# Kernel tuning notes

Measured on AMD Instinct MI355X. Metric: run time of the kernel, lower is better.

Reference implementation:

```python
import math
import jax, jax.numpy as jnp
import numpy as np

VOCAB, D, H, L, DFF, MAXLEN, PAD = 32000, 512, 8, 6, 2048, 5000, 0
DK = D // H
EPS = 1e-5


def _positional_encoding(max_len, d_model):
    pos = np.arange(max_len, dtype=np.float32)[:, None]
    div = np.exp(np.arange(0, d_model, 2, dtype=np.float32) * (-math.log(10000.0) / d_model))
    pe = np.zeros((max_len, d_model), dtype=np.float32)
    pe[:, 0::2] = np.sin(pos * div)
    pe[:, 1::2] = np.cos(pos * div)
    return jnp.asarray(pe)


def setup_inputs() -> dict:
    key = jax.random.key(0)
    ks = jax.random.split(key, 16)
    B, S = 2, 2048
    src = jax.random.randint(ks[0], (B, S), 0, VOCAB)
    emb = jax.random.normal(ks[1], (VOCAB, D), jnp.float32) * (D ** -0.5)
    emb = emb.at[PAD].set(0.0)  # padding_idx row zeroed
    pe = _positional_encoding(MAXLEN, D)
    s = 0.02
    WQ = jax.random.normal(ks[2], (L, D, D), jnp.float32) * s
    WK = jax.random.normal(ks[3], (L, D, D), jnp.float32) * s
    WV = jax.random.normal(ks[4], (L, D, D), jnp.float32) * s
    WO = jax.random.normal(ks[5], (L, D, D), jnp.float32) * s
    W1 = jax.random.normal(ks[6], (L, D, DFF), jnp.float32) * s
    b1 = jnp.zeros((L, DFF), jnp.float32)
    W2 = jax.random.normal(ks[7], (L, DFF, D), jnp.float32) * s
    b2 = jnp.zeros((L, D), jnp.float32)
    ln1_s = jnp.ones((L, D), jnp.float32); ln1_b = jnp.zeros((L, D), jnp.float32)
    ln2_s = jnp.ones((L, D), jnp.float32); ln2_b = jnp.zeros((L, D), jnp.float32)
    fn_s = jnp.ones((D,), jnp.float32); fn_b = jnp.zeros((D,), jnp.float32)
    return dict(src=src, emb=emb, pe=pe, WQ=WQ, WK=WK, WV=WV, WO=WO,
                W1=W1, b1=b1, W2=W2, b2=b2, ln1_s=ln1_s, ln1_b=ln1_b,
                ln2_s=ln2_s, ln2_b=ln2_b, fn_s=fn_s, fn_b=fn_b)


def _layernorm(x, scale, bias):
    mu = jnp.mean(x, axis=-1, keepdims=True)
    var = jnp.mean(jnp.square(x - mu), axis=-1, keepdims=True)
    return (x - mu) * jax.lax.rsqrt(var + EPS) * scale + bias


def _encoder_forward(src, emb, pe, WQ, WK, WV, WO, W1, b1, W2, b2,
                     ln1_s, ln1_b, ln2_s, ln2_b, fn_s, fn_b):
    B, S = src.shape
    key_mask = (src != PAD)[:, None, None, :]  # [B,1,1,S] padding mask
    x = emb[src] * math.sqrt(D) + pe[:S]        # [B,S,D] (dropout=eval/off)
    for l in range(L):
        # --- pre-LN self-attention ---
        h = _layernorm(x, ln1_s[l], ln1_b[l])
        q = (h @ WQ[l]).reshape(B, S, H, DK).transpose(0, 2, 1, 3)
        k = (h @ WK[l]).reshape(B, S, H, DK).transpose(0, 2, 1, 3)
        v = (h @ WV[l]).reshape(B, S, H, DK).transpose(0, 2, 1, 3)
        scores = jnp.einsum('bhqd,bhkd->bhqk', q, k) / math.sqrt(DK)
        scores = jnp.where(key_mask, scores, -jnp.inf)
        w = jax.nn.softmax(scores, axis=-1)
        w = jnp.nan_to_num(w, nan=0.0)
        attn = jnp.einsum('bhqk,bhkd->bhqd', w, v)
        attn = attn.transpose(0, 2, 1, 3).reshape(B, S, D) @ WO[l]
        x = x + attn
        # --- pre-LN FFN ---
        h = _layernorm(x, ln2_s[l], ln2_b[l])
        h = jax.nn.relu(h @ W1[l] + b1[l]) @ W2[l] + b2[l]
        x = x + h
    return _layernorm(x, fn_s, fn_b)


def reference(src, emb, pe, WQ, WK, WV, WO, W1, b1, W2, b2,
              ln1_s, ln1_b, ln2_s, ln2_b, fn_s, fn_b):
    return _encoder_forward(src, emb, pe, WQ, WK, WV, WO, W1, b1, W2, b2,
                            ln1_s, ln1_b, ln2_s, ln2_b, fn_s, fn_b)
```

## Files before the change

### kernel.cpp

```cpp
#include <hip/hip_runtime.h>


typedef _Float16 f16;
typedef _Float16 f16x8 __attribute__((ext_vector_type(8)));
typedef _Float16 f16x4 __attribute__((ext_vector_type(4)));
typedef float    f32x4 __attribute__((ext_vector_type(4)));

#define MFMA16(a, b, c) __builtin_amdgcn_mfma_f32_16x16x32_f16((a), (b), (c), 0, 0, 0)
#define GLOAD_LDS16(GP, LP)                                        \
  __builtin_amdgcn_global_load_lds(                                \
      (const __attribute__((address_space(1))) void*)(GP),         \
      (__attribute__((address_space(3))) void*)(LP), 16, 0, 0)

__device__ inline float fast_exp2(float x) {
#if __has_builtin(__builtin_amdgcn_exp2f)
  return __builtin_amdgcn_exp2f(x);
#else
  return exp2f(x);
#endif
}

static constexpr int Dm  = 512;
static constexpr int Sx  = 2048;
static constexpr int NTOK = 4096;
static constexpr int DFFm = 2048;
static constexpr int Lc  = 6;

__global__ __launch_bounds__(256) void transpose_qkvo(
    const float* __restrict__ WQ, const float* __restrict__ WK,
    const float* __restrict__ WV, const float* __restrict__ WO,
    f16* __restrict__ wqkv, f16* __restrict__ wtO)
{
  __shared__ float t[32][33];
  const int z = blockIdx.z;
  const int widx = z / 6, layer = z % 6;
  const float* src = ((widx == 0) ? WQ : (widx == 1) ? WK : (widx == 2) ? WV : WO)
                     + (size_t)layer * Dm * Dm;
  f16* dst = (widx < 3)
      ? wqkv + (size_t)layer * 1536 * Dm + (size_t)widx * 512 * Dm
      : wtO + (size_t)layer * Dm * Dm;
  const int r0 = blockIdx.y * 32, c0 = blockIdx.x * 32;
  const int tx = threadIdx.x, ty = threadIdx.y;
  #pragma unroll
  for (int i = 0; i < 4; i++)
    t[ty + i * 8][tx] = src[(size_t)(r0 + ty + i * 8) * Dm + c0 + tx];
  __syncthreads();
  #pragma unroll
  for (int i = 0; i < 4; i++)
    dst[(size_t)(c0 + ty + i * 8) * Dm + r0 + tx] = (f16)t[tx][ty + i * 8];
}

__global__ __launch_bounds__(256) void transpose_cvt(
    const float* __restrict__ in, f16* __restrict__ out, int R, int C, size_t zs)
{
  __shared__ float t[32][33];
  const int z = blockIdx.z;
  const float* src = in + (size_t)z * zs;
  f16* dst = out + (size_t)z * zs;
  const int r0 = blockIdx.y * 32, c0 = blockIdx.x * 32;
  const int tx = threadIdx.x, ty = threadIdx.y;
  #pragma unroll
  for (int i = 0; i < 4; i++)
    t[ty + i * 8][tx] = src[(size_t)(r0 + ty + i * 8) * C + c0 + tx];
  __syncthreads();
  #pragma unroll
  for (int i = 0; i < 4; i++)
    dst[(size_t)(c0 + ty + i * 8) * R + r0 + tx] = (f16)t[tx][ty + i * 8];
}

__global__ __launch_bounds__(256) void embed_k(
    const int* __restrict__ src, const float* __restrict__ emb,
    const float* __restrict__ pe, float* __restrict__ x, float* __restrict__ mb)
{
  const int gid = blockIdx.x * 256 + threadIdx.x;
  const int token = gid >> 6;
  const int d0 = (gid & 63) << 3;
  const int s = token & (Sx - 1);
  const int tk = src[token];
  if ((gid & 63) == 0) mb[token] = (tk != 0) ? 0.f : -3.0e38f;
  const float* e = emb + (size_t)tk * Dm + d0;
  const float* p = pe + (size_t)s * Dm + d0;
  float* o = x + (size_t)token * Dm + d0;
  const float SC = 22.627416997969522f;
  #pragma unroll
  for (int j = 0; j < 8; j++) o[j] = e[j] * SC + p[j];
}

template <typename OUT, int ADD, int BIAS, int WRITEX>
__global__ __launch_bounds__(256) void lnf_k(
    const float* __restrict__ x, const f16* __restrict__ part,
    const float* __restrict__ bias,
    const float* __restrict__ sc, const float* __restrict__ bi,
    OUT* __restrict__ out, float* __restrict__ xout)
{
  const int row = blockIdx.x * 4 + (threadIdx.x >> 6);
  const int l = threadIdx.x & 63;
  const float* px = x + (size_t)row * Dm + l * 8;
  float v[8];
  *(float4*)&v[0] = *(const float4*)px;
  *(float4*)&v[4] = *(const float4*)(px + 4);
  if constexpr (ADD) {
    f16x8 p = *(const f16x8*)(part + (size_t)row * Dm + l * 8);
    #pragma unroll
    for (int j = 0; j < 8; j++) v[j] += (float)p[j];
    if constexpr (BIAS) {
      float bb[8];
      *(float4*)&bb[0] = *(const float4*)(bias + l * 8);
      *(float4*)&bb[4] = *(const float4*)(bias + l * 8 + 4);
      #pragma unroll
      for (int j = 0; j < 8; j++) v[j] += bb[j];
    }
    if constexpr (WRITEX) {
      float* pxo = xout + (size_t)row * Dm + l * 8;
      *(float4*)pxo = *(const float4*)&v[0];
      *(float4*)(pxo + 4) = *(const float4*)&v[4];
    }
  }
  float s = 0.f;
  #pragma unroll
  for (int j = 0; j < 8; j++) s += v[j];
  #pragma unroll
  for (int m = 1; m < 64; m <<= 1) s += __shfl_xor(s, m);
  const float mu = s * (1.0f / 512.0f);
  float qv = 0.f;
  #pragma unroll
  for (int j = 0; j < 8; j++) { float d = v[j] - mu; qv += d * d; }
  #pragma unroll
  for (int m = 1; m < 64; m <<= 1) qv += __shfl_xor(qv, m);
  const float inv = rsqrtf(qv * (1.0f / 512.0f) + 1e-5f);
  float scv[8], biv[8];
  *(float4*)&scv[0] = *(const float4*)(sc + l * 8);
  *(float4*)&scv[4] = *(const float4*)(sc + l * 8 + 4);
  *(float4*)&biv[0] = *(const float4*)(bi + l * 8);
  *(float4*)&biv[4] = *(const float4*)(bi + l * 8 + 4);
  if constexpr (sizeof(OUT) == 2) {
    f16x8 o;
    #pragma unroll
    for (int j = 0; j < 8; j++) o[j] = (f16)((v[j] - mu) * inv * scv[j] + biv[j]);
    *(f16x8*)((f16*)out + (size_t)row * Dm + l * 8) = o;
  } else {
    float o[8];
    #pragma unroll
    for (int j = 0; j < 8; j++) o[j] = (v[j] - mu) * inv * scv[j] + biv[j];
    float* po = (float*)out + (size_t)row * Dm + l * 8;
    *(float4*)po = *(float4*)&o[0];
    *(float4*)(po + 4) = *(float4*)&o[4];
  }
}

template <int BN, int MODE, int N, int K>
__global__ __launch_bounds__(256) void gemm_k(
    const f16* __restrict__ A, const f16* __restrict__ Bt,
    f16* __restrict__ O0, f16* __restrict__ O1, f16* __restrict__ O2,
    const float* __restrict__ bias)
{
  constexpr int BM = 128;
  constexpr int NF = (BN >= 32) ? BN / 32 : 1;
  constexpr int NBM = NTOK / BM;
  constexpr int NBN = N / BN;
  constexpr int NB = NBM * NBN;
  __shared__ f16 lsA[2][BM * 64];
  __shared__ f16 lsB[2][BN * 64];
  const int tid = threadIdx.x;
  const int l = tid & 63, w = tid >> 6;
  const int lr = l & 15, lh = l >> 4;
  const int wm = w >> 1, wn = w & 1;
  const int bid = blockIdx.x;
  const int nid = (bid & 7) * (NB / 8) + (bid >> 3);
  const int bm = nid / NBN, bn = nid % NBN;

  constexpr int ACH = (BM * 64) / (256 * 8);
  constexpr int BCH = (BN * 64) / (256 * 8);
  const size_t rowA0 = (size_t)bm * BM;
  const size_t rowB0 = (size_t)bn * BN;

  auto stage = [&](int kt, int pb) {
    #pragma unroll
    for (int i = 0; i < ACH; i++) {
      int c = i * 256 + tid, r = c >> 3, g = c & 7, gs = g ^ (r & 7);
      GLOAD_LDS16(A + (rowA0 + r) * K + kt * 64 + gs * 8, &lsA[pb][c * 8]);
    }
    #pragma unroll
    for (int i = 0; i < BCH; i++) {
      int c = i * 256 + tid, r = c >> 3, g = c & 7, gs = g ^ (r & 7);
      GLOAD_LDS16(Bt + (rowB0 + r) * K + kt * 64 + gs * 8, &lsB[pb][c * 8]);
    }
  };

  f32x4 acc[4][NF] = {};
  stage(0, 0);
  constexpr int NT = K >> 6;
  for (int kt = 0; kt < NT; ++kt) {
    const int cur = kt & 1;
    __syncthreads();
    if (kt + 1 < NT) stage(kt + 1, cur ^ 1);
    #pragma unroll
    for (int s = 0; s < 2; s++) {
      const int gg = (s * 4 + lh) ^ (lr & 7);
      f16x8 af[4], bf[NF];
      #pragma unroll
      for (int mf = 0; mf < 4; mf++)
        af[mf] = *(const f16x8*)(&lsA[cur][(wm * 64 + mf * 16 + lr) * 64 + gg * 8]);
      #pragma unroll
      for (int nf = 0; nf < NF; nf++)
        bf[nf] = *(const f16x8*)(&lsB[cur][(wn * (BN / 2) + nf * 16 + lr) * 64 + gg * 8]);
      #pragma unroll
      for (int mf = 0; mf < 4; mf++)
        #pragma unroll
        for (int nf = 0; nf < NF; nf++)
          acc[mf][nf] = MFMA16(af[mf], bf[nf], acc[mf][nf]);
    }
  }

  #pragma unroll
  for (int mf = 0; mf < 4; mf++) {
    #pragma unroll
    for (int nf = 0; nf < NF; nf++) {
      const int token = bm * BM + wm * 64 + mf * 16 + lh * 4;
      const int ch = bn * BN + wn * (BN / 2) + nf * 16 + lr;
      if constexpr (MODE == 0) {
        const int part = ch >> 9;
        const int pch = ch & 511;
        if (part == 2) {
          f16x4 o;
          #pragma unroll
          for (int r = 0; r < 4; r++) o[r] = (f16)acc[mf][nf][r];
          const int bb = token >> 11, ss = token & (Sx - 1);
          const int scol = (ss & ~31) | (((ss >> 2) & 3) << 3) | (((ss >> 4) & 1) << 2);
          *(f16x4*)(O2 + ((size_t)((bb << 3) + (pch >> 6)) * 64 + (pch & 63)) * Sx + scol) = o;
        } else {
          f16* Oz = (part == 0) ? O0 : O1;
          #pragma unroll
          for (int r = 0; r < 4; r++)
            Oz[(size_t)(token + r) * Dm + pch] = (f16)acc[mf][nf][r];
        }
      } else if constexpr (MODE == 1) {
        #pragma unroll
        for (int r = 0; r < 4; r++)
          O0[(size_t)(token + r) * N + ch] = (f16)acc[mf][nf][r];
      } else {
        #pragma unroll
        for (int r = 0; r < 4; r++) {
          float v = acc[mf][nf][r] + bias[ch];
          O0[(size_t)(token + r) * N + ch] = (f16)fmaxf(v, 0.f);
        }
      }
    }
  }
}

__global__ __launch_bounds__(512) void attn_k(
    const f16* __restrict__ q, const f16* __restrict__ kk,
    const f16* __restrict__ vt, const float* __restrict__ maskb,
    f16* __restrict__ out)
{
  __shared__ f16 lsK[2][2][64 * 64];
  __shared__ f16 lsV[2][2][64 * 64];
  const int tid = threadIdx.x;
  const int l = tid & 63, w = tid >> 6;
  const int lr = l & 15, lh = l >> 4;
  const int grp = w >> 2;
  const int t256 = tid & 255;
  const int bid = blockIdx.x;
  const int nid = ((bid & 7) << 6) + (bid >> 3);
  const int bh = nid >> 5;
  const int qt = nid & 31;
  const int b = bh >> 3, h = bh & 7;

  const _Float16 QS = (_Float16)0.18033688f;
  f16x8 qf[2];
  #pragma unroll
  for (int s = 0; s < 2; s++) {
    size_t row = (size_t)(b * Sx + qt * 64 + (w & 3) * 16 + lr);
    f16x8 t = *(const f16x8*)(q + row * Dm + h * 64 + s * 32 + lh * 8);
    qf[s] = t * QS;
  }

  const f16x8 ones = {(f16)1, (f16)1, (f16)1, (f16)1,
                      (f16)1, (f16)1, (f16)1, (f16)1};
  f32x4 oacc[4] = {};
  f32x4 sumacc = {};
  float mrun = -1e30f;

  auto stage = [&](int t, int pb) {
    #pragma unroll
    for (int i = 0; i < 2; i++) {
      int c = i * 256 + t256, r = c >> 3, g = c & 7, gs = g ^ (r & 7);
      GLOAD_LDS16(kk + (size_t)(b * Sx + t * 64 + r) * Dm + h * 64 + gs * 8,
                  &lsK[grp][pb][c * 8]);
      GLOAD_LDS16(vt + (size_t)(bh * 64 + r) * Sx + t * 64 + gs * 8,
                  &lsV[grp][pb][c * 8]);
    }
  };
  stage(grp * 16, 0);

  for (int i = 0; i < 16; ++i) {
    const int t = grp * 16 + i;
    const int cur = i & 1;
    __syncthreads();
    if (i < 15) stage(t + 1, cur ^ 1);

    f32x4 sacc[4];
    #pragma unroll
    for (int kf = 0; kf < 4; kf++)
      sacc[kf] = *(const f32x4*)(maskb + b * Sx + t * 64 + kf * 16 + lh * 4);
    __builtin_amdgcn_s_setprio(1);
    #pragma unroll
    for (int s = 0; s < 2; s++) {
      const int gk = (s * 4 + lh) ^ (lr & 7);
      #pragma unroll
      for (int kf = 0; kf < 4; kf++) {
        f16x8 a = *(const f16x8*)(&lsK[grp][cur][(kf * 16 + lr) * 64 + gk * 8]);
        sacc[kf] = MFMA16(a, qf[s], sacc[kf]);
      }
    }
    __builtin_amdgcn_s_setprio(0);

    float pmax;
    {
      float t0 = fmaxf(fmaxf(sacc[0][0], sacc[0][1]), sacc[0][2]);
      float t1 = fmaxf(fmaxf(sacc[0][3], sacc[1][0]), sacc[1][1]);
      float t2 = fmaxf(fmaxf(sacc[1][2], sacc[1][3]), sacc[2][0]);
      float t3 = fmaxf(fmaxf(sacc[2][1], sacc[2][2]), sacc[2][3]);
      float t4 = fmaxf(fmaxf(sacc[3][0], sacc[3][1]), sacc[3][2]);
      float u0 = fmaxf(fmaxf(t0, t1), sacc[3][3]);
      float u1 = fmaxf(fmaxf(t2, t3), t4);
      pmax = fmaxf(u0, u1);
    }
    pmax = fmaxf(pmax, __shfl_xor(pmax, 16));
    pmax = fmaxf(pmax, __shfl_xor(pmax, 32));
    if (!__all(pmax - mrun <= 8.0f)) {
      const float mnew = fmaxf(mrun, pmax);
      const float rs = fast_exp2(mrun - mnew);
      sumacc *= rs;
      #pragma unroll
      for (int mf = 0; mf < 4; mf++) oacc[mf] *= rs;
      mrun = mnew;
    }
    #pragma unroll
    for (int kf = 0; kf < 4; kf++)
      #pragma unroll
      for (int r = 0; r < 4; r++)
        sacc[kf][r] = fast_exp2(sacc[kf][r] - mrun);
    f16x8 pa[2];
    #pragma unroll
    for (int s = 0; s < 2; s++)
      #pragma unroll
      for (int jj = 0; jj < 8; jj++)
        pa[s][jj] = (f16)sacc[2 * s + (jj >> 2)][jj & 3];
    sumacc = MFMA16(ones, pa[0], sumacc);
    sumacc = MFMA16(ones, pa[1], sumacc);

    __builtin_amdgcn_s_setprio(1);
    #pragma unroll
    for (int s = 0; s < 2; s++) {
      const int gv = (4 * s + lh) ^ (lr & 7);
      #pragma unroll
      for (int mf = 0; mf < 4; mf++) {
        f16x8 vv = *(const f16x8*)(&lsV[grp][cur][(mf * 16 + lr) * 64 + gv * 8]);
        oacc[mf] = MFMA16(vv, pa[s], oacc[mf]);
      }
    }
    __builtin_amdgcn_s_setprio(0);
  }

  const float lrun = sumacc[0];
  __syncthreads();
  float* sO  = (float*)&lsK[0][0][0];
  float* sML = (float*)&lsV[0][0][0];
  const int wl = (w & 3) * 64 + l;
  if (grp == 1) {
    #pragma unroll
    for (int mf = 0; mf < 4; mf++)
      #pragma unroll
      for (int r = 0; r < 4; r++) sO[wl * 16 + mf * 4 + r] = oacc[mf][r];
    sML[wl * 2] = mrun;
    sML[wl * 2 + 1] = lrun;
  }
  __syncthreads();
  if (grp == 0) {
    const float m1 = sML[wl * 2], l1 = sML[wl * 2 + 1];
    const float mm = fmaxf(mrun, m1);
    const float s0 = fast_exp2(mrun - mm), s1 = fast_exp2(m1 - mm);
    const float inv = 1.f / (lrun * s0 + l1 * s1);
    size_t row = (size_t)(b * Sx + qt * 64 + (w & 3) * 16 + lr);
    #pragma unroll
    for (int mf = 0; mf < 4; mf++) {
      f16x4 o;
      #pragma unroll
      for (int r = 0; r < 4; r++)
        o[r] = (f16)((oacc[mf][r] * s0 + sO[wl * 16 + mf * 4 + r] * s1) * inv);
      *(f16x4*)(out + row * Dm + h * 64 + mf * 16 + lh * 4) = o;
    }
  }
}

extern "C" void kernel_launch(void* const* d_in, const int* in_sizes, int n_in,
                              void* d_out, int out_size, void* d_ws, size_t ws_size,
                              hipStream_t stream)
{
  (void)in_sizes; (void)n_in; (void)out_size; (void)ws_size;
  const int*   src  = (const int*)d_in[0];
  const float* emb  = (const float*)d_in[1];
  const float* pe   = (const float*)d_in[2];
  const float* WQ   = (const float*)d_in[3];
  const float* WK   = (const float*)d_in[4];
  const float* WV   = (const float*)d_in[5];
  const float* WO   = (const float*)d_in[6];
  const float* W1   = (const float*)d_in[7];
  const float* b1   = (const float*)d_in[8];
  const float* W2   = (const float*)d_in[9];
  const float* b2   = (const float*)d_in[10];
  const float* ln1s = (const float*)d_in[11];
  const float* ln1b = (const float*)d_in[12];
  const float* ln2s = (const float*)d_in[13];
  const float* ln2b = (const float*)d_in[14];
  const float* fns  = (const float*)d_in[15];
  const float* fnb  = (const float*)d_in[16];

  char* ws = (char*)d_ws;
  const size_t DD = (size_t)Dm * Dm;
  const size_t DQKV = (size_t)1536 * Dm;
  const size_t DF = (size_t)Dm * DFFm;
  f16* wqkv = (f16*)(ws);
  f16* wtO  = wqkv + Lc * DQKV;
  f16* wt1  = wtO + Lc * DD;
  f16* wt2  = wt1 + Lc * DF;
  float* x  = (float*)(wt2 + Lc * DF);
  f16* hbuf = (f16*)(x + (size_t)NTOK * Dm);
  f16* qb   = hbuf + (size_t)NTOK * Dm;
  f16* kb   = qb + (size_t)NTOK * Dm;
  f16* vtb  = kb + (size_t)NTOK * Dm;
  f16* attn = vtb + (size_t)NTOK * Dm;
  f16* aout = attn + (size_t)NTOK * Dm;
  f16* ff   = aout + (size_t)NTOK * Dm;
  f16* ffo  = ff + (size_t)NTOK * DFFm;
  float* maskb = (float*)(ffo + (size_t)NTOK * Dm);

  const dim3 tb(32, 8);
  transpose_qkvo<<<dim3(16, 16, 24), tb, 0, stream>>>(WQ, WK, WV, WO, wqkv, wtO);
  transpose_cvt<<<dim3(64, 16, Lc), tb, 0, stream>>>(W1, wt1, Dm, DFFm, DF);
  transpose_cvt<<<dim3(16, 64, Lc), tb, 0, stream>>>(W2, wt2, DFFm, Dm, DF);

  embed_k<<<1024, 256, 0, stream>>>(src, emb, pe, x, maskb);

  for (int l = 0; l < Lc; l++) {
    const f16* wqkv_l = wqkv + (size_t)l * DQKV;
    const f16* wo = wtO + (size_t)l * DD;
    const f16* w1 = wt1 + (size_t)l * DF;
    const f16* w2 = wt2 + (size_t)l * DF;

    if (l == 0)
      lnf_k<f16, 0, 0, 0><<<1024, 256, 0, stream>>>(
          x, nullptr, nullptr, ln1s, ln1b, hbuf, nullptr);
    else
      lnf_k<f16, 1, 1, 1><<<1024, 256, 0, stream>>>(
          x, ffo, b2 + (size_t)(l - 1) * Dm, ln1s + l * Dm, ln1b + l * Dm,
          hbuf, x);
    gemm_k<64, 0, 1536, 512><<<768, 256, 0, stream>>>(
        hbuf, wqkv_l, qb, kb, vtb, nullptr);
    attn_k<<<512, 512, 0, stream>>>(qb, kb, vtb, maskb, attn);
    gemm_k<32, 1, 512, 512><<<512, 256, 0, stream>>>(
        attn, wo, aout, nullptr, nullptr, nullptr);
    lnf_k<f16, 1, 0, 1><<<1024, 256, 0, stream>>>(
        x, aout, nullptr, ln2s + l * Dm, ln2b + l * Dm, hbuf, x);
    gemm_k<128, 2, 2048, 512><<<512, 256, 0, stream>>>(
        hbuf, w1, ff, nullptr, nullptr, b1 + (size_t)l * DFFm);
    gemm_k<32, 1, 512, 2048><<<512, 256, 0, stream>>>(
        ff, w2, ffo, nullptr, nullptr, nullptr);
  }

  lnf_k<float, 1, 1, 0><<<1024, 256, 0, stream>>>(
      x, ffo, b2 + (size_t)(Lc - 1) * Dm, fns, fnb, (float*)d_out, x);
}
```

Baseline: 666.3 us.

## Split-K FFN2 GEMM with fused partial sum; restructure attention to 4 KV groups

The W2 GEMM now uses split-K=2 with BN=64, writing two f16 partial outputs that the following layernorm kernel sums, so it is no longer a long K=2048 loop. The attention kernel is reorganized so each warp handles 32 queries (two 16-row fragments), with four KV groups of 8 tiles each merged at the end instead of two groups of 16. Double-buffered K/V staging is dropped in favour of load-then-sync. This adds extra partial traffic and an extra f16 rounding of partials, and removes load/compute overlap in attention.

Result: slower. 713.3 us (+7.1%).

```diff
diff --git a/kernel.cpp b/kernel.cpp
--- a/kernel.cpp
+++ b/kernel.cpp
@@ -89,7 +89,7 @@
 template <typename OUT, int ADD, int BIAS, int WRITEX>
 __global__ __launch_bounds__(256) void lnf_k(
     const float* __restrict__ x, const f16* __restrict__ part,
-    const float* __restrict__ bias,
+    const f16* __restrict__ part2, const float* __restrict__ bias,
     const float* __restrict__ sc, const float* __restrict__ bi,
     OUT* __restrict__ out, float* __restrict__ xout)
 {
@@ -99,10 +99,15 @@
   float v[8];
   *(float4*)&v[0] = *(const float4*)px;
   *(float4*)&v[4] = *(const float4*)(px + 4);
-  if constexpr (ADD) {
+  if constexpr (ADD >= 1) {
     f16x8 p = *(const f16x8*)(part + (size_t)row * Dm + l * 8);
     #pragma unroll
     for (int j = 0; j < 8; j++) v[j] += (float)p[j];
+    if constexpr (ADD == 2) {
+      f16x8 p2 = *(const f16x8*)(part2 + (size_t)row * Dm + l * 8);
+      #pragma unroll
+      for (int j = 0; j < 8; j++) v[j] += (float)p2[j];
+    }
     if constexpr (BIAS) {
       float bb[8];
       *(float4*)&bb[0] = *(const float4*)(bias + l * 8);
@@ -148,7 +153,7 @@
   }
 }
 
-template <int BN, int MODE, int N, int K>
+template <int BN, int MODE, int N, int K, int SK>
 __global__ __launch_bounds__(256) void gemm_k(
     const f16* __restrict__ A, const f16* __restrict__ Bt,
     f16* __restrict__ O0, f16* __restrict__ O1, f16* __restrict__ O2,
@@ -158,7 +163,7 @@
   constexpr int NF = (BN >= 32) ? BN / 32 : 1;
   constexpr int NBM = NTOK / BM;
   constexpr int NBN = N / BN;
-  constexpr int NB = NBM * NBN;
+  constexpr int NB = NBM * NBN * SK;
   __shared__ f16 lsA[2][BM * 64];
   __shared__ f16 lsB[2][BN * 64];
   const int tid = threadIdx.x;
@@ -167,29 +172,32 @@
   const int wm = w >> 1, wn = w & 1;
   const int bid = blockIdx.x;
   const int nid = (bid & 7) * (NB / 8) + (bid >> 3);
-  const int bm = nid / NBN, bn = nid % NBN;
+  const int ks = nid / (NBM * NBN);
+  const int rr = nid % (NBM * NBN);
+  const int bm = rr / NBN, bn = rr % NBN;
 
   constexpr int ACH = (BM * 64) / (256 * 8);
   constexpr int BCH = (BN * 64) / (256 * 8);
   const size_t rowA0 = (size_t)bm * BM;
   const size_t rowB0 = (size_t)bn * BN;
+  const int k0 = ks * (K / SK);
 
   auto stage = [&](int kt, int pb) {
     #pragma unroll
     for (int i = 0; i < ACH; i++) {
       int c = i * 256 + tid, r = c >> 3, g = c & 7, gs = g ^ (r & 7);
-      GLOAD_LDS16(A + (rowA0 + r) * K + kt * 64 + gs * 8, &lsA[pb][c * 8]);
+      GLOAD_LDS16(A + (rowA0 + r) * K + k0 + kt * 64 + gs * 8, &lsA[pb][c * 8]);
     }
     #pragma unroll
     for (int i = 0; i < BCH; i++) {
       int c = i * 256 + tid, r = c >> 3, g = c & 7, gs = g ^ (r & 7);
-      GLOAD_LDS16(Bt + (rowB0 + r) * K + kt * 64 + gs * 8, &lsB[pb][c * 8]);
+      GLOAD_LDS16(Bt + (rowB0 + r) * K + k0 + kt * 64 + gs * 8, &lsB[pb][c * 8]);
     }
   };
 
   f32x4 acc[4][NF] = {};
   stage(0, 0);
-  constexpr int NT = K >> 6;
+  constexpr int NT = (K / SK) >> 6;
   for (int kt = 0; kt < NT; ++kt) {
     const int cur = kt & 1;
     __syncthreads();
@@ -238,12 +246,17 @@
         #pragma unroll
         for (int r = 0; r < 4; r++)
           O0[(size_t)(token + r) * N + ch] = (f16)acc[mf][nf][r];
-      } else {
+      } else if constexpr (MODE == 2) {
         #pragma unroll
         for (int r = 0; r < 4; r++) {
           float v = acc[mf][nf][r] + bias[ch];
           O0[(size_t)(token + r) * N + ch] = (f16)fmaxf(v, 0.f);
         }
+      } else {
+        f16* dst = O0 + (size_t)ks * NTOK * N;
+        #pragma unroll
+        for (int r = 0; r < 4; r++)
+          dst[(size_t)(token + r) * N + ch] = (f16)acc[mf][nf][r];
       }
     }
   }
@@ -254,13 +267,14 @@
     const f16* __restrict__ vt, const float* __restrict__ maskb,
     f16* __restrict__ out)
 {
-  __shared__ f16 lsK[2][2][64 * 64];
-  __shared__ f16 lsV[2][2][64 * 64];
+  __shared__ f16 lds[32768];
+  f16* lsK = lds;
+  f16* lsV = lds + 16384;
   const int tid = threadIdx.x;
   const int l = tid & 63, w = tid >> 6;
   const int lr = l & 15, lh = l >> 4;
-  const int grp = w >> 2;
-  const int t256 = tid & 255;
+  const int grp = w >> 1, wq = w & 1;
+  const int t128 = tid & 127;
   const int bid = blockIdx.x;
   const int nid = ((bid & 7) << 6) + (bid >> 3);
   const int bh = nid >> 5;
@@ -268,88 +282,96 @@
   const int b = bh >> 3, h = bh & 7;
 
   const _Float16 QS = (_Float16)0.18033688f;
-  f16x8 qf[2];
-  #pragma unroll
-  for (int s = 0; s < 2; s++) {
-    size_t row = (size_t)(b * Sx + qt * 64 + (w & 3) * 16 + lr);
-    f16x8 t = *(const f16x8*)(q + row * Dm + h * 64 + s * 32 + lh * 8);
-    qf[s] = t * QS;
-  }
+  f16x8 qf[2][2];
+  #pragma unroll
+  for (int s = 0; s < 2; s++)
+    #pragma unroll
+    for (int j = 0; j < 2; j++) {
+      size_t row = (size_t)(b * Sx + qt * 64 + wq * 32 + j * 16 + lr);
+      f16x8 t = *(const f16x8*)(q + row * Dm + h * 64 + s * 32 + lh * 8);
+      qf[s][j] = t * QS;
+    }
 
   const f16x8 ones = {(f16)1, (f16)1, (f16)1, (f16)1,
                       (f16)1, (f16)1, (f16)1, (f16)1};
-  f32x4 oacc[4] = {};
-  f32x4 sumacc = {};
-  float mrun = -1e30f;
-
-  auto stage = [&](int t, int pb) {
-    #pragma unroll
-    for (int i = 0; i < 2; i++) {
-      int c = i * 256 + t256, r = c >> 3, g = c & 7, gs = g ^ (r & 7);
+  f32x4 oacc[4][2] = {};
+  f32x4 sumacc[2] = {};
+  float mrun[2] = {-1e30f, -1e30f};
+
+  auto stage = [&](int t) {
+    #pragma unroll
+    for (int i = 0; i < 4; i++) {
+      int c = i * 128 + t128, r = c >> 3, g = c & 7, gs = g ^ (r & 7);
       GLOAD_LDS16(kk + (size_t)(b * Sx + t * 64 + r) * Dm + h * 64 + gs * 8,
-                  &lsK[grp][pb][c * 8]);
+                  lsK + grp * 4096 + c * 8);
       GLOAD_LDS16(vt + (size_t)(bh * 64 + r) * Sx + t * 64 + gs * 8,
-                  &lsV[grp][pb][c * 8]);
+                  lsV + grp * 4096 + c * 8);
     }
   };
-  stage(grp * 16, 0);
-
-  for (int i = 0; i < 16; ++i) {
-    const int t = grp * 16 + i;
-    const int cur = i & 1;
+
+  for (int i = 0; i < 8; ++i) {
+    const int t = grp * 8 + i;
     __syncthreads();
-    if (i < 15) stage(t + 1, cur ^ 1);
-
-    f32x4 sacc[4];
-    #pragma unroll
-    for (int kf = 0; kf < 4; kf++)
-      sacc[kf] = *(const f32x4*)(maskb + b * Sx + t * 64 + kf * 16 + lh * 4);
+    stage(t);
+    __syncthreads();
+
+    f32x4 sacc[4][2];
+    #pragma unroll
+    for (int kf = 0; kf < 4; kf++) {
+      f32x4 mv = *(const f32x4*)(maskb + b * Sx + t * 64 + kf * 16 + lh * 4);
+      sacc[kf][0] = mv;
+      sacc[kf][1] = mv;
+    }
     __builtin_amdgcn_s_setprio(1);
     #pragma unroll
     for (int s = 0; s < 2; s++) {
       const int gk = (s * 4 + lh) ^ (lr & 7);
       #pragma unroll
       for (int kf = 0; kf < 4; kf++) {
-        f16x8 a = *(const f16x8*)(&lsK[grp][cur][(kf * 16 + lr) * 64 + gk * 8]);
-        sacc[kf] = MFMA16(a, qf[s], sacc[kf]);
+        f16x8 a = *(const f16x8*)(lsK + grp * 4096 + (kf * 16 + lr) * 64 + gk * 8);
+        sacc[kf][0] = MFMA16(a, qf[s][0], sacc[kf][0]);
+        sacc[kf][1] = MFMA16(a, qf[s][1], sacc[kf][1]);
       }
     }
     __builtin_amdgcn_s_setprio(0);
 
-    float pmax;
-    {
-      float t0 = fmaxf(fmaxf(sacc[0][0], sacc[0][1]), sacc[0][2]);
-      float t1 = fmaxf(fmaxf(sacc[0][3], sacc[1][0]), sacc[1][1]);
-      float t2 = fmaxf(fmaxf(sacc[1][2], sacc[1][3]), sacc[2][0]);
-      float t3 = fmaxf(fmaxf(sacc[2][1], sacc[2][2]), sacc[2][3]);
-      float t4 = fmaxf(fmaxf(sacc[3][0], sacc[3][1]), sacc[3][2]);
-      float u0 = fmaxf(fmaxf(t0, t1), sacc[3][3]);
-      float u1 = fmaxf(fmaxf(t2, t3), t4);
-      pmax = fmaxf(u0, u1);
-    }
-    pmax = fmaxf(pmax, __shfl_xor(pmax, 16));
-    pmax = fmaxf(pmax, __shfl_xor(pmax, 32));
-    if (!__all(pmax - mrun <= 8.0f)) {
-      const float mnew = fmaxf(mrun, pmax);
-      const float rs = fast_exp2(mrun - mnew);
-      sumacc *= rs;
-      #pragma unroll
-      for (int mf = 0; mf < 4; mf++) oacc[mf] *= rs;
-      mrun = mnew;
-    }
-    #pragma unroll
-    for (int kf = 0; kf < 4; kf++)
-      #pragma unroll
-      for (int r = 0; r < 4; r++)
-        sacc[kf][r] = fast_exp2(sacc[kf][r] - mrun);
-    f16x8 pa[2];
-    #pragma unroll
-    for (int s = 0; s < 2; s++)
-      #pragma unroll
-      for (int jj = 0; jj < 8; jj++)
-        pa[s][jj] = (f16)sacc[2 * s + (jj >> 2)][jj & 3];
-    sumacc = MFMA16(ones, pa[0], sumacc);
-    sumacc = MFMA16(ones, pa[1], sumacc);
+    f16x8 pa[2][2];
+    #pragma unroll
+    for (int j = 0; j < 2; j++) {
+      float pmax;
+      {
+        float t0 = fmaxf(fmaxf(sacc[0][j][0], sacc[0][j][1]), sacc[0][j][2]);
+        float t1 = fmaxf(fmaxf(sacc[0][j][3], sacc[1][j][0]), sacc[1][j][1]);
+        float t2 = fmaxf(fmaxf(sacc[1][j][2], sacc[1][j][3]), sacc[2][j][0]);
+        float t3 = fmaxf(fmaxf(sacc[2][j][1], sacc[2][j][2]), sacc[2][j][3]);
+        float t4 = fmaxf(fmaxf(sacc[3][j][0], sacc[3][j][1]), sacc[3][j][2]);
+        float u0 = fmaxf(fmaxf(t0, t1), sacc[3][j][3]);
+        float u1 = fmaxf(fmaxf(t2, t3), t4);
+        pmax = fmaxf(u0, u1);
+      }
+      pmax = fmaxf(pmax, __shfl_xor(pmax, 16));
+      pmax = fmaxf(pmax, __shfl_xor(pmax, 32));
+      if (!__all(pmax - mrun[j] <= 8.0f)) {
+        const float mnew = fmaxf(mrun[j], pmax);
+        const float rs = fast_exp2(mrun[j] - mnew);
+        sumacc[j] *= rs;
+        #pragma unroll
+        for (int mf = 0; mf < 4; mf++) oacc[mf][j] *= rs;
+        mrun[j] = mnew;
+      }
+      #pragma unroll
+      for (int kf = 0; kf < 4; kf++)
+        #pragma unroll
+        for (int r = 0; r < 4; r++)
+          sacc[kf][j][r] = fast_exp2(sacc[kf][j][r] - mrun[j]);
+      #pragma unroll
+      for (int s = 0; s < 2; s++)
+        #pragma unroll
+        for (int jj = 0; jj < 8; jj++)
+          pa[s][j][jj] = (f16)sacc[2 * s + (jj >> 2)][j][jj & 3];
+      sumacc[j] = MFMA16(ones, pa[0][j], sumacc[j]);
+      sumacc[j] = MFMA16(ones, pa[1][j], sumacc[j]);
+    }
 
     __builtin_amdgcn_s_setprio(1);
     #pragma unroll
@@ -357,40 +379,61 @@
       const int gv = (4 * s + lh) ^ (lr & 7);
       #pragma unroll
       for (int mf = 0; mf < 4; mf++) {
-        f16x8 vv = *(const f16x8*)(&lsV[grp][cur][(mf * 16 + lr) * 64 + gv * 8]);
-        oacc[mf] = MFMA16(vv, pa[s], oacc[mf]);
+        f16x8 vv = *(const f16x8*)(lsV + grp * 4096 + (mf * 16 + lr) * 64 + gv * 8);
+        oacc[mf][0] = MFMA16(vv, pa[s][0], oacc[mf][0]);
+        oacc[mf][1] = MFMA16(vv, pa[s][1], oacc[mf][1]);
       }
     }
     __builtin_amdgcn_s_setprio(0);
   }
 
-  const float lrun = sumacc[0];
+  const float lrun[2] = {sumacc[0][0], sumacc[1][0]};
   __syncthreads();
-  float* sO  = (float*)&lsK[0][0][0];
-  float* sML = (float*)&lsV[0][0][0];
-  const int wl = (w & 3) * 64 + l;
-  if (grp == 1) {
-    #pragma unroll
-    for (int mf = 0; mf < 4; mf++)
-      #pragma unroll
-      for (int r = 0; r < 4; r++) sO[wl * 16 + mf * 4 + r] = oacc[mf][r];
-    sML[wl * 2] = mrun;
-    sML[wl * 2 + 1] = lrun;
+  float* sO  = (float*)lds;
+  float* sML = (float*)(lds + 28672);
+  if (grp != 0) {
+    #pragma unroll
+    for (int j = 0; j < 2; j++) {
+      const int qq = wq * 32 + j * 16 + lr;
+      #pragma unroll
+      for (int mf = 0; mf < 4; mf++)
+        *(f32x4*)&sO[((grp - 1) * 64 + qq) * 64 + mf * 16 + lh * 4] = oacc[mf][j];
+      sML[(grp - 1) * 128 + qq * 2]     = mrun[j];
+      sML[(grp - 1) * 128 + qq * 2 + 1] = lrun[j];
+    }
   }
   __syncthreads();
   if (grp == 0) {
-    const float m1 = sML[wl * 2], l1 = sML[wl * 2 + 1];
-    const float mm = fmaxf(mrun, m1);
-    const float s0 = fast_exp2(mrun - mm), s1 = fast_exp2(m1 - mm);
-    const float inv = 1.f / (lrun * s0 + l1 * s1);
-    size_t row = (size_t)(b * Sx + qt * 64 + (w & 3) * 16 + lr);
-    #pragma unroll
-    for (int mf = 0; mf < 4; mf++) {
-      f16x4 o;
-      #pragma unroll
-      for (int r = 0; r < 4; r++)
-        o[r] = (f16)((oacc[mf][r] * s0 + sO[wl * 16 + mf * 4 + r] * s1) * inv);
-      *(f16x4*)(out + row * Dm + h * 64 + mf * 16 + lh * 4) = o;
+    #pragma unroll
+    for (int j = 0; j < 2; j++) {
+      const int qq = wq * 32 + j * 16 + lr;
+      float mg[3], lg[3];
+      #pragma unroll
+      for (int g = 0; g < 3; g++) {
+        mg[g] = sML[g * 128 + qq * 2];
+        lg[g] = sML[g * 128 + qq * 2 + 1];
+      }
+      float mm = fmaxf(fmaxf(mrun[j], mg[0]), fmaxf(mg[1], mg[2]));
+      const float s0 = fast_exp2(mrun[j] - mm);
+      float sg[3];
+      #pragma unroll
+      for (int g = 0; g < 3; g++) sg[g] = fast_exp2(mg[g] - mm);
+      const float inv = 1.f /
+          (lrun[j] * s0 + lg[0] * sg[0] + lg[1] * sg[1] + lg[2] * sg[2]);
+      size_t row = (size_t)(b * Sx + qt * 64 + wq * 32 + j * 16 + lr);
+      #pragma unroll
+      for (int mf = 0; mf < 4; mf++) {
+        f16x4 o;
+        #pragma unroll
+        for (int r = 0; r < 4; r++) {
+          float v = oacc[mf][j][r] * s0;
+          #pragma unroll
+          for (int g = 0; g < 3; g++)
+            v += sO[(g * 64 + qq) * 64 + mf * 16 + lh * 4 + r] * sg[g];
+          o[r] = (f16)(v * inv);
+        }
+        *(f16x4*)(out + row * Dm + h * 64 + mf * 16 + lh * 4) = o;
+      }
     }
   }
 }
@@ -435,7 +478,7 @@
   f16* aout = attn + (size_t)NTOK * Dm;
   f16* ff   = aout + (size_t)NTOK * Dm;
   f16* ffo  = ff + (size_t)NTOK * DFFm;
-  float* maskb = (float*)(ffo + (size_t)NTOK * Dm);
+  float* maskb = (float*)(ffo + (size_t)2 * NTOK * Dm);
 
   const dim3 tb(32, 8);
   transpose_qkvo<<<dim3(16, 16, 24), tb, 0, stream>>>(WQ, WK, WV, WO, wqkv, wtO);
@@ -444,6 +487,7 @@
 
   embed_k<<<1024, 256, 0, stream>>>(src, emb, pe, x, maskb);
 
+  f16* ffo1 = ffo + (size_t)NTOK * Dm;
   for (int l = 0; l < Lc; l++) {
     const f16* wqkv_l = wqkv + (size_t)l * DQKV;
     const f16* wo = wtO + (size_t)l * DD;
@@ -452,24 +496,24 @@
 
     if (l == 0)
       lnf_k<f16, 0, 0, 0><<<1024, 256, 0, stream>>>(
-          x, nullptr, nullptr, ln1s, ln1b, hbuf, nullptr);
+          x, nullptr, nullptr, nullptr, ln1s, ln1b, hbuf, nullptr);
     else
-      lnf_k<f16, 1, 1, 1><<<1024, 256, 0, stream>>>(
-          x, ffo, b2 + (size_t)(l - 1) * Dm, ln1s + l * Dm, ln1b + l * Dm,
+      lnf_k<f16, 2, 1, 1><<<1024, 256, 0, stream>>>(
+          x, ffo, ffo1, b2 + (size_t)(l - 1) * Dm, ln1s + l * Dm, ln1b + l * Dm,
           hbuf, x);
-    gemm_k<64, 0, 1536, 512><<<768, 256, 0, stream>>>(
+    gemm_k<64, 0, 1536, 512, 1><<<768, 256, 0, stream>>>(
         hbuf, wqkv_l, qb, kb, vtb, nullptr);
     attn_k<<<512, 512, 0, stream>>>(qb, kb, vtb, maskb, attn);
-    gemm_k<32, 1, 512, 512><<<512, 256, 0, stream>>>(
+    gemm_k<32, 1, 512, 512, 1><<<512, 256, 0, stream>>>(
         attn, wo, aout, nullptr, nullptr, nullptr);
     lnf_k<f16, 1, 0, 1><<<1024, 256, 0, stream>>>(
-        x, aout, nullptr, ln2s + l * Dm, ln2b + l * Dm, hbuf, x);
-    gemm_k<128, 2, 2048, 512><<<512, 256, 0, stream>>>(
+        x, aout, nullptr, nullptr, ln2s + l * Dm, ln2b + l * Dm, hbuf, x);
+    gemm_k<128, 2, 2048, 512, 1><<<512, 256, 0, stream>>>(
         hbuf, w1, ff, nullptr, nullptr, b1 + (size_t)l * DFFm);
-    gemm_k<32, 1, 512, 2048><<<512, 256, 0, stream>>>(
+    gemm_k<64, 3, 512, 2048, 2><<<512, 256, 0, stream>>>(
         ff, w2, ffo, nullptr, nullptr, nullptr);
   }
 
-  lnf_k<float, 1, 1, 0><<<1024, 256, 0, stream>>>(
-      x, ffo, b2 + (size_t)(Lc - 1) * Dm, fns, fnb, (float*)d_out, x);
-}
+  lnf_k<float, 2, 1, 0><<<1024, 256, 0, stream>>>(
+      x, ffo, ffo1, b2 + (size_t)(Lc - 1) * Dm, fns, fnb, (float*)d_out, x);
+}
```

## Split-K the FFN down-projection GEMM and fold partial sums into layernorm

Applied to the files above, without the earlier changes.

The W2 GEMM (K=2048) now uses split-K with two K halves and a wider N tile (BN=64), writing two fp16 partial outputs into separate buffers. The following layernorm kernel gains an ADD==2 mode that sums both partials along with the residual and bias. The aim is to keep the same block count while halving each block's K loop and raising per-block MFMA work per tile. The cost is an extra fp16 partial buffer written and read, and an extra fp16 rounding of each partial sum.

Result: faster. 623.6 us (-6.4%).

```diff
diff --git a/kernel.cpp b/kernel.cpp
--- a/kernel.cpp
+++ b/kernel.cpp
@@ -89,7 +89,7 @@
 template <typename OUT, int ADD, int BIAS, int WRITEX>
 __global__ __launch_bounds__(256) void lnf_k(
     const float* __restrict__ x, const f16* __restrict__ part,
-    const float* __restrict__ bias,
+    const f16* __restrict__ part2, const float* __restrict__ bias,
     const float* __restrict__ sc, const float* __restrict__ bi,
     OUT* __restrict__ out, float* __restrict__ xout)
 {
@@ -99,10 +99,15 @@
   float v[8];
   *(float4*)&v[0] = *(const float4*)px;
   *(float4*)&v[4] = *(const float4*)(px + 4);
-  if constexpr (ADD) {
+  if constexpr (ADD >= 1) {
     f16x8 p = *(const f16x8*)(part + (size_t)row * Dm + l * 8);
     #pragma unroll
     for (int j = 0; j < 8; j++) v[j] += (float)p[j];
+    if constexpr (ADD == 2) {
+      f16x8 p2 = *(const f16x8*)(part2 + (size_t)row * Dm + l * 8);
+      #pragma unroll
+      for (int j = 0; j < 8; j++) v[j] += (float)p2[j];
+    }
     if constexpr (BIAS) {
       float bb[8];
       *(float4*)&bb[0] = *(const float4*)(bias + l * 8);
@@ -148,7 +153,7 @@
   }
 }
 
-template <int BN, int MODE, int N, int K>
+template <int BN, int MODE, int N, int K, int SK>
 __global__ __launch_bounds__(256) void gemm_k(
     const f16* __restrict__ A, const f16* __restrict__ Bt,
     f16* __restrict__ O0, f16* __restrict__ O1, f16* __restrict__ O2,
@@ -158,7 +163,7 @@
   constexpr int NF = (BN >= 32) ? BN / 32 : 1;
   constexpr int NBM = NTOK / BM;
   constexpr int NBN = N / BN;
-  constexpr int NB = NBM * NBN;
+  constexpr int NB = NBM * NBN * SK;
   __shared__ f16 lsA[2][BM * 64];
   __shared__ f16 lsB[2][BN * 64];
   const int tid = threadIdx.x;
@@ -167,29 +172,32 @@
   const int wm = w >> 1, wn = w & 1;
   const int bid = blockIdx.x;
   const int nid = (bid & 7) * (NB / 8) + (bid >> 3);
-  const int bm = nid / NBN, bn = nid % NBN;
+  const int ks = nid / (NBM * NBN);
+  const int rr = nid % (NBM * NBN);
+  const int bm = rr / NBN, bn = rr % NBN;
 
   constexpr int ACH = (BM * 64) / (256 * 8);
   constexpr int BCH = (BN * 64) / (256 * 8);
   const size_t rowA0 = (size_t)bm * BM;
   const size_t rowB0 = (size_t)bn * BN;
+  const int k0 = ks * (K / SK);
 
   auto stage = [&](int kt, int pb) {
     #pragma unroll
     for (int i = 0; i < ACH; i++) {
       int c = i * 256 + tid, r = c >> 3, g = c & 7, gs = g ^ (r & 7);
-      GLOAD_LDS16(A + (rowA0 + r) * K + kt * 64 + gs * 8, &lsA[pb][c * 8]);
+      GLOAD_LDS16(A + (rowA0 + r) * K + k0 + kt * 64 + gs * 8, &lsA[pb][c * 8]);
     }
     #pragma unroll
     for (int i = 0; i < BCH; i++) {
       int c = i * 256 + tid, r = c >> 3, g = c & 7, gs = g ^ (r & 7);
-      GLOAD_LDS16(Bt + (rowB0 + r) * K + kt * 64 + gs * 8, &lsB[pb][c * 8]);
+      GLOAD_LDS16(Bt + (rowB0 + r) * K + k0 + kt * 64 + gs * 8, &lsB[pb][c * 8]);
     }
   };
 
   f32x4 acc[4][NF] = {};
   stage(0, 0);
-  constexpr int NT = K >> 6;
+  constexpr int NT = (K / SK) >> 6;
   for (int kt = 0; kt < NT; ++kt) {
     const int cur = kt & 1;
     __syncthreads();
@@ -238,12 +246,17 @@
         #pragma unroll
         for (int r = 0; r < 4; r++)
           O0[(size_t)(token + r) * N + ch] = (f16)acc[mf][nf][r];
-      } else {
+      } else if constexpr (MODE == 2) {
         #pragma unroll
         for (int r = 0; r < 4; r++) {
           float v = acc[mf][nf][r] + bias[ch];
           O0[(size_t)(token + r) * N + ch] = (f16)fmaxf(v, 0.f);
         }
+      } else {
+        f16* dst = O0 + (size_t)ks * NTOK * N;
+        #pragma unroll
+        for (int r = 0; r < 4; r++)
+          dst[(size_t)(token + r) * N + ch] = (f16)acc[mf][nf][r];
       }
     }
   }
@@ -435,7 +448,7 @@
   f16* aout = attn + (size_t)NTOK * Dm;
   f16* ff   = aout + (size_t)NTOK * Dm;
   f16* ffo  = ff + (size_t)NTOK * DFFm;
-  float* maskb = (float*)(ffo + (size_t)NTOK * Dm);
+  float* maskb = (float*)(ffo + (size_t)2 * NTOK * Dm);
 
   const dim3 tb(32, 8);
   transpose_qkvo<<<dim3(16, 16, 24), tb, 0, stream>>>(WQ, WK, WV, WO, wqkv, wtO);
@@ -444,6 +457,7 @@
 
   embed_k<<<1024, 256, 0, stream>>>(src, emb, pe, x, maskb);
 
+  f16* ffo1 = ffo + (size_t)NTOK * Dm;
   for (int l = 0; l < Lc; l++) {
     const f16* wqkv_l = wqkv + (size_t)l * DQKV;
     const f16* wo = wtO + (size_t)l * DD;
@@ -452,24 +466,24 @@
 
     if (l == 0)
       lnf_k<f16, 0, 0, 0><<<1024, 256, 0, stream>>>(
-          x, nullptr, nullptr, ln1s, ln1b, hbuf, nullptr);
+          x, nullptr, nullptr, nullptr, ln1s, ln1b, hbuf, nullptr);
     else
-      lnf_k<f16, 1, 1, 1><<<1024, 256, 0, stream>>>(
-          x, ffo, b2 + (size_t)(l - 1) * Dm, ln1s + l * Dm, ln1b + l * Dm,
+      lnf_k<f16, 2, 1, 1><<<1024, 256, 0, stream>>>(
+          x, ffo, ffo1, b2 + (size_t)(l - 1) * Dm, ln1s + l * Dm, ln1b + l * Dm,
           hbuf, x);
-    gemm_k<64, 0, 1536, 512><<<768, 256, 0, stream>>>(
+    gemm_k<64, 0, 1536, 512, 1><<<768, 256, 0, stream>>>(
         hbuf, wqkv_l, qb, kb, vtb, nullptr);
     attn_k<<<512, 512, 0, stream>>>(qb, kb, vtb, maskb, attn);
-    gemm_k<32, 1, 512, 512><<<512, 256, 0, stream>>>(
+    gemm_k<32, 1, 512, 512, 1><<<512, 256, 0, stream>>>(
         attn, wo, aout, nullptr, nullptr, nullptr);
     lnf_k<f16, 1, 0, 1><<<1024, 256, 0, stream>>>(
-        x, aout, nullptr, ln2s + l * Dm, ln2b + l * Dm, hbuf, x);
-    gemm_k<128, 2, 2048, 512><<<512, 256, 0, stream>>>(
+        x, aout, nullptr, nullptr, ln2s + l * Dm, ln2b + l * Dm, hbuf, x);
+    gemm_k<128, 2, 2048, 512, 1><<<512, 256, 0, stream>>>(
         hbuf, w1, ff, nullptr, nullptr, b1 + (size_t)l * DFFm);
-    gemm_k<32, 1, 512, 2048><<<512, 256, 0, stream>>>(
+    gemm_k<64, 3, 512, 2048, 2><<<512, 256, 0, stream>>>(
         ff, w2, ffo, nullptr, nullptr, nullptr);
   }
 
-  lnf_k<float, 1, 1, 0><<<1024, 256, 0, stream>>>(
-      x, ffo, b2 + (size_t)(Lc - 1) * Dm, fns, fnb, (float*)d_out, x);
-}
+  lnf_k<float, 2, 1, 0><<<1024, 256, 0, stream>>>(
+      x, ffo, ffo1, b2 + (size_t)(Lc - 1) * Dm, fns, fnb, (float*)d_out, x);
+}
```
